# Optimization experiments

Measured on AMD Instinct MI355X. Metric: run time of the kernel, lower is better.

## Reference

```python
import jax, jax.numpy as jnp
import numpy as np

# e3nn normalize2mom constants: 1/sqrt(E[act(z)^2]) for z ~ N(0,1)
_z = np.random.default_rng(0).standard_normal(1_000_000)
_C_SILU = np.float32(1.0 / np.sqrt(np.mean((_z / (1.0 + np.exp(-_z))) ** 2)))
_C_SIGMOID = np.float32(1.0 / np.sqrt(np.mean((1.0 / (1.0 + np.exp(-_z))) ** 2)))

E = 131072
MUL0, MUL1 = 256, 128          # node irreps: 256x0e + 128x1e
RBF = 64
W_NUMEL = 256 + 256 + 128 + 128  # uvu weights in instruction order: A,C,B,D
INV_SQRT3 = np.float32(1.0 / np.sqrt(3.0))
INV_SQRT2 = np.float32(1.0 / np.sqrt(2.0))
INV_SQRT_FAN = np.float32(1.0 / np.sqrt(384.0))  # LinearRS rescale (fan_in=384)


def setup_inputs() -> dict:
    key = jax.random.key(0)
    ks = jax.random.split(key, 8)
    f32 = jnp.float32
    return {
        "node_input": jax.random.normal(ks[0], (E, MUL0 + MUL1 * 3), f32),
        "edge_attr": jax.random.normal(ks[1], (E, 4), f32),        # sh: 1x0e + 1x1e
        "edge_scalars": jax.random.normal(ks[2], (E, RBF), f32),
        "rad_w1": jax.random.normal(ks[3], (RBF, 64), f32) / np.float32(np.sqrt(RBF)),
        "rad_ln_g": jnp.ones((64,), f32),
        "rad_ln_b": jnp.zeros((64,), f32),
        "rad_w2": jax.random.normal(ks[4], (64, W_NUMEL), f32) / np.float32(8.0),
        "rad_offset": jnp.zeros((W_NUMEL,), f32),
        "lin_w0": jax.random.normal(ks[5], (384, 384), f32),
        "lin_b0": jnp.zeros((384,), f32),
        "lin_w1": jax.random.normal(ks[6], (384, MUL1), f32),
    }


def reference(node_input, edge_attr, edge_scalars, rad_w1, rad_ln_g, rad_ln_b,
              rad_w2, rad_offset, lin_w0, lin_b0, lin_w1):
    # --- RadialProfile: Linear(no bias) -> LayerNorm -> SiLU -> Linear(no bias) + offset
    h = edge_scalars @ rad_w1
    mu = jnp.mean(h, axis=-1, keepdims=True)
    var = jnp.var(h, axis=-1, keepdims=True)
    h = (h - mu) * jax.lax.rsqrt(var + 1e-5) * rad_ln_g + rad_ln_b
    h = jax.nn.silu(h)
    w = h @ rad_w2 + rad_offset                        # [E, 768] per-edge DTP weights
    wA, wC, wB, wD = w[:, :256], w[:, 256:512], w[:, 512:640], w[:, 640:]

    x0 = node_input[:, :MUL0]                          # [E,256]  0e
    x1 = node_input[:, MUL0:].reshape(-1, MUL1, 3)     # [E,128,3] 1e
    sh0 = edge_attr[:, 0:1]                            # [E,1]
    sh1 = edge_attr[:, 1:4]                            # [E,3]

    # --- DepthwiseTensorProduct ('uvu', path_weight = sqrt(dim(ir_out)), w3j orthonormal)
    outA = x0 * sh0 * wA                                                # 0e x 0e -> 0e [E,256]
    outB = jnp.einsum('eui,ei->eu', x1, sh1) * INV_SQRT3 * wB           # 1e . 1e -> 0e [E,128]
    outC = (x0 * wC)[:, :, None] * sh1[:, None, :]                      # 0e x 1e -> 1e [E,256,3]
    outD = jnp.cross(x1, sh1[:, None, :]) * INV_SQRT2 * wD[:, :, None]  # 1e x 1e -> 1e [E,128,3]

    d0 = jnp.concatenate([outA, outB], axis=-1)        # [E,384]   0e block (sorted irreps)
    d1 = jnp.concatenate([outC, outD], axis=1)         # [E,384,3] 1e block

    # --- LinearRS: per-irrep linear with 1/sqrt(fan_in) rescale; bias on 0e only
    out0 = d0 @ lin_w0 * INV_SQRT_FAN + lin_b0                       # [E,384] = 256 scalars + 128 gates
    out1 = jnp.einsum('eum,uv->evm', d1, lin_w1) * INV_SQRT_FAN      # [E,128,3] gated 1e

    # --- Gate: normalize2mom(SiLU) on scalars, normalize2mom(sigmoid) gates on 1e
    scalars = _C_SILU * jax.nn.silu(out0[:, :MUL0])
    gates = _C_SIGMOID * jax.nn.sigmoid(out0[:, MUL0:])
    gated = out1 * gates[:, :, None]
    return jnp.concatenate([scalars, gated.reshape(gated.shape[0], -1)], axis=-1)  # [E,640]
```

## Files before the change

### kernel.cpp

```cpp
#include <hip/hip_runtime.h>
#include <stdint.h>

typedef __attribute__((ext_vector_type(8))) short short8;
typedef __attribute__((ext_vector_type(4))) float f32x4;

#define OW1R  0
#define OW2R  4096
#define OW0T  53248
#define OW1CT 200704
#define OW1DT 233472

#define OATTR 0
#define OES   512
#define OHS   4608
#define OD0   8704
#define OH    8704
#define OZC   33280
#define OZD0  49664
#define SMEM_BYTES 74240

static constexpr float C_SILU      = 1.6765390f;
static constexpr float C_SIG       = 1.8462240f;
static constexpr float INV_SQRT3   = 0.5773502691896258f;
static constexpr float INV_SQRT2   = 0.7071067811865476f;
static constexpr float INV_SQRT_FAN= 0.051031036307982884f;

__device__ __forceinline__ short f2bf(float f) {
  union { float f; uint32_t u; } v; v.f = f;
  uint32_t u = v.u;
  u += 0x7FFFu + ((u >> 16) & 1u);
  return (short)(u >> 16);
}

__device__ __forceinline__ f32x4 mfma16(short8 a, short8 b, f32x4 c) {
  return __builtin_amdgcn_mfma_f32_16x16x32_bf16(a, b, c, 0, 0, 0);
}

__device__ __forceinline__ short8 ldF(const short* __restrict__ W, int nkt, int nt, int kt, int lane) {
  return *(const short8*)(W + ((((nt * nkt) + kt) << 6) + lane) * 8);
}

__global__ void prep_weights(const float* __restrict__ rw1, const float* __restrict__ rw2,
                             const float* __restrict__ lw0, const float* __restrict__ lw1,
                             short* __restrict__ ws)
{
  int idx = blockIdx.x * blockDim.x + threadIdx.x;
  int stride = gridDim.x * blockDim.x;
  for (int i = idx; i < 4096; i += stride) {
    int e = i & 7, lane = (i >> 3) & 63, f = i >> 9;
    int kt = f & 1, nt = f >> 1;
    int n = nt * 16 + (lane & 15), k = kt * 32 + ((lane >> 4) << 3) + e;
    ws[OW1R + i] = f2bf(rw1[k * 64 + n]);
  }
  for (int i = idx; i < 49152; i += stride) {
    int e = i & 7, lane = (i >> 3) & 63, f = i >> 9;
    int kt = f & 1, nt = f >> 1;
    int n = nt * 16 + (lane & 15), k = kt * 32 + ((lane >> 4) << 3) + e;
    ws[OW2R + i] = f2bf(rw2[k * 768 + n]);
  }
  for (int i = idx; i < 147456; i += stride) {
    int e = i & 7, lane = (i >> 3) & 63, f = i >> 9;
    int kt = f % 12, nt = f / 12;
    int n = nt * 16 + (lane & 15), k = kt * 32 + ((lane >> 4) << 3) + e;
    ws[OW0T + i] = f2bf(lw0[k * 384 + n] * INV_SQRT_FAN);
  }
  for (int i = idx; i < 32768; i += stride) {
    int e = i & 7, lane = (i >> 3) & 63, f = i >> 9;
    int kt = f & 7, nt = f >> 3;
    int n = nt * 16 + (lane & 15), k = kt * 32 + ((lane >> 4) << 3) + e;
    ws[OW1CT + i] = f2bf(lw1[k * 128 + n] * INV_SQRT_FAN);
  }
  for (int i = idx; i < 16384; i += stride) {
    int e = i & 7, lane = (i >> 3) & 63, f = i >> 9;
    int kt = f & 3, nt = f >> 2;
    int n = nt * 16 + (lane & 15), k = kt * 32 + ((lane >> 4) << 3) + e;
    ws[OW1DT + i] = f2bf(lw1[(256 + k) * 128 + n] * INV_SQRT_FAN);
  }
}

#define SWZ(row, byte) ((byte) ^ ((((row) & 7) << 4) ^ (((row) & 8) << 2)))
#define LDA(base, c2, row, k0) \
  (*(const short8*)(smem + (base) + (row) * (c2) + SWZ(row, (k0) << 1)))
#define STBF(base, c2, row, col, val) \
  (*(short*)(smem + (base) + (row) * (c2) + SWZ(row, (col) << 1)) = f2bf(val))

__global__ __launch_bounds__(256) void fctp_fused(
    const float* __restrict__ node, const float* __restrict__ eattr,
    const float* __restrict__ escal, const float* __restrict__ lng,
    const float* __restrict__ lnb, const float* __restrict__ roff,
    const float* __restrict__ b0v, const short* __restrict__ ws,
    float* __restrict__ out)
{
  __shared__ char smem[SMEM_BYTES];
  const int t = threadIdx.x;
  const int lane = t & 63;
  const int w = t >> 6;
  const int row0 = blockIdx.x << 5;
  const int l15 = lane & 15;
  const int kof = (lane >> 4) << 3;
  const int rb0 = (lane >> 4) << 2;

  float attr_v = 0.f;
  if (t < 128) attr_v = eattr[(size_t)row0 * 4 + t];
  const int pr = t >> 3, pc0 = (t & 7) << 3;
  const float* pesc = escal + (size_t)(row0 + pr) * 64 + pc0;
  float4 ev0 = *(const float4*)pesc;
  float4 ev1 = *(const float4*)(pesc + 4);

  float4 lg0 = *(const float4*)(lng + pc0);
  float4 lg1 = *(const float4*)(lng + pc0 + 4);
  float4 lb0 = *(const float4*)(lnb + pc0);
  float4 lb1 = *(const float4*)(lnb + pc0 + 4);

  float offAr[4], offCr[4], offBr[2], offDr[2];
#pragma unroll
  for (int j = 0; j < 4; ++j) {
    int u = (((w << 2) + j) << 4) + l15;
    offAr[j] = roff[u];
    offCr[j] = roff[256 + u];
  }
#pragma unroll
  for (int j = 0; j < 2; ++j) {
    int u = (((w << 1) + j) << 4) + l15;
    offBr[j] = roff[512 + u];
    offDr[j] = roff[640 + u];
  }

  float x0r[4][2][4];
#pragma unroll
  for (int j = 0; j < 4; ++j) {
    int u = (((w << 2) + j) << 4) + l15;
#pragma unroll
    for (int rt = 0; rt < 2; ++rt)
#pragma unroll
      for (int i = 0; i < 4; ++i)
        x0r[j][rt][i] = node[(size_t)(row0 + rt * 16 + rb0 + i) * 640 + u];
  }
  float x1r[2][2][4][3];
#pragma unroll
  for (int j = 0; j < 2; ++j) {
    int u = (((w << 1) + j) << 4) + l15;
#pragma unroll
    for (int rt = 0; rt < 2; ++rt)
#pragma unroll
      for (int i = 0; i < 4; ++i) {
        const float* xp = node + (size_t)(row0 + rt * 16 + rb0 + i) * 640 + 256 + u * 3;
        x1r[j][rt][i][0] = xp[0];
        x1r[j][rt][i][1] = xp[1];
        x1r[j][rt][i][2] = xp[2];
      }
  }

  {
    if (t < 128) ((float*)(smem + OATTR))[t] = attr_v;
    short8 bv;
    bv[0] = f2bf(ev0.x); bv[1] = f2bf(ev0.y); bv[2] = f2bf(ev0.z); bv[3] = f2bf(ev0.w);
    bv[4] = f2bf(ev1.x); bv[5] = f2bf(ev1.y); bv[6] = f2bf(ev1.z); bv[7] = f2bf(ev1.w);
    *(short8*)(smem + OES + pr * 128 + SWZ(pr, pc0 << 1)) = bv;
  }
  __syncthreads();

  {
    short8 bf0 = ldF(ws + OW1R, 2, w, 0, lane);
    short8 bf1 = ldF(ws + OW1R, 2, w, 1, lane);
    float* sh_h = (float*)(smem + OH);
    int colh = (w << 4) + l15;
#pragma unroll
    for (int rt = 0; rt < 2; ++rt) {
      int r = rt * 16 + l15;
      f32x4 acc = {0.f, 0.f, 0.f, 0.f};
      acc = mfma16(LDA(OES, 128, r, kof), bf0, acc);
      acc = mfma16(LDA(OES, 128, r, 32 + kof), bf1, acc);
      int rb = rt * 16 + rb0;
#pragma unroll
      for (int i = 0; i < 4; ++i) sh_h[(rb + i) * 68 + colh] = acc[i];
    }
  }
  __syncthreads();

  {
    const float* sh_h = (const float*)(smem + OH);
    float vals[8]; float s = 0.f, s2 = 0.f;
#pragma unroll
    for (int j = 0; j < 8; ++j) {
      float v = sh_h[pr * 68 + pc0 + j];
      vals[j] = v; s += v; s2 += v * v;
    }
#pragma unroll
    for (int off = 1; off < 8; off <<= 1) {
      s  += __shfl_xor(s, off, 64);
      s2 += __shfl_xor(s2, off, 64);
    }
    float mu = s * 0.015625f;
    float var = s2 * 0.015625f - mu * mu;
    float rstd = rsqrtf(var + 1e-5f);
    float lg[8] = {lg0.x, lg0.y, lg0.z, lg0.w, lg1.x, lg1.y, lg1.z, lg1.w};
    float lb[8] = {lb0.x, lb0.y, lb0.z, lb0.w, lb1.x, lb1.y, lb1.z, lb1.w};
    short8 hv;
#pragma unroll
    for (int j = 0; j < 8; ++j) {
      float v = (vals[j] - mu) * rstd * lg[j] + lb[j];
      float sv = v / (1.f + __expf(-v));
      hv[j] = f2bf(sv);
    }
    *(short8*)(smem + OHS + pr * 128 + SWZ(pr, pc0 << 1)) = hv;
  }
  __syncthreads();

  {
    const float* attr = (const float*)(smem + OATTR);
    float s0r[2][4], sar[2][4], sbr[2][4], scr[2][4];
#pragma unroll
    for (int rt = 0; rt < 2; ++rt)
#pragma unroll
      for (int i = 0; i < 4; ++i) {
        int row = rt * 16 + rb0 + i;
        s0r[rt][i] = attr[row * 4 + 0];
        sar[rt][i] = attr[row * 4 + 1];
        sbr[rt][i] = attr[row * 4 + 2];
        scr[rt][i] = attr[row * 4 + 3];
      }
    short8 a00 = LDA(OHS, 128, l15, kof);
    short8 a01 = LDA(OHS, 128, l15, 32 + kof);
    short8 a10 = LDA(OHS, 128, 16 + l15, kof);
    short8 a11 = LDA(OHS, 128, 16 + l15, 32 + kof);

#pragma unroll
    for (int j = 0; j < 4; ++j) {
      int ut = (w << 2) + j;
      short8 bA0 = ldF(ws + OW2R, 2, ut, 0, lane);
      short8 bA1 = ldF(ws + OW2R, 2, ut, 1, lane);
      short8 bC0 = ldF(ws + OW2R, 2, ut + 16, 0, lane);
      short8 bC1 = ldF(ws + OW2R, 2, ut + 16, 1, lane);
      int u = (ut << 4) + l15;
#pragma unroll
      for (int rt = 0; rt < 2; ++rt) {
        short8 fa = rt ? a10 : a00, fb = rt ? a11 : a01;
        f32x4 accA = {0.f,0.f,0.f,0.f}, accC = {0.f,0.f,0.f,0.f};
        accA = mfma16(fa, bA0, accA); accA = mfma16(fb, bA1, accA);
        accC = mfma16(fa, bC0, accC); accC = mfma16(fb, bC1, accC);
#pragma unroll
        for (int i = 0; i < 4; ++i) {
          int row = rt * 16 + rb0 + i;
          float x0v = x0r[j][rt][i];
          STBF(OD0, 768, row, u, x0v * s0r[rt][i] * (accA[i] + offAr[j]));
          STBF(OZC, 512, row, u, x0v * (accC[i] + offCr[j]));
        }
      }
    }
#pragma unroll
    for (int j = 0; j < 2; ++j) {
      int ut = (w << 1) + j;
      short8 bB0 = ldF(ws + OW2R, 2, 32 + ut, 0, lane);
      short8 bB1 = ldF(ws + OW2R, 2, 32 + ut, 1, lane);
      short8 bD0 = ldF(ws + OW2R, 2, 40 + ut, 0, lane);
      short8 bD1 = ldF(ws + OW2R, 2, 40 + ut, 1, lane);
      int u = (ut << 4) + l15;
#pragma unroll
      for (int rt = 0; rt < 2; ++rt) {
        short8 fa = rt ? a10 : a00, fb = rt ? a11 : a01;
        f32x4 accB = {0.f,0.f,0.f,0.f}, accD = {0.f,0.f,0.f,0.f};
        accB = mfma16(fa, bB0, accB); accB = mfma16(fb, bB1, accB);
        accD = mfma16(fa, bD0, accD); accD = mfma16(fb, bD1, accD);
#pragma unroll
        for (int i = 0; i < 4; ++i) {
          int row = rt * 16 + rb0 + i;
          float xa = x1r[j][rt][i][0], xb = x1r[j][rt][i][1], xc = x1r[j][rt][i][2];
          float sa = sar[rt][i], sb = sbr[rt][i], sc = scr[rt][i];
          float wB = accB[i] + offBr[j], wD = accD[i] + offDr[j];
          STBF(OD0, 768, row, 256 + u,
               (xa * sa + xb * sb + xc * sc) * INV_SQRT3 * wB);
          float zd = wD * INV_SQRT2;
          STBF(OZD0,          256, row, u, xa * zd);
          STBF(OZD0 + 8192,   256, row, u, xb * zd);
          STBF(OZD0 + 16384,  256, row, u, xc * zd);
        }
      }
    }
  }
  __syncthreads();


#pragma unroll
  for (int cp = 0; cp < 2; ++cp) {
    f32x4 sacc[2][2];
#pragma unroll
    for (int q = 0; q < 2; ++q)
#pragma unroll
      for (int rt = 0; rt < 2; ++rt) sacc[q][rt] = (f32x4){0.f, 0.f, 0.f, 0.f};
#pragma unroll
    for (int kt = 0; kt < 12; ++kt) {
      int k0 = kt * 32 + kof;
      short8 Af0 = LDA(OD0, 768, l15, k0);
      short8 Af1 = LDA(OD0, 768, 16 + l15, k0);
      short8 Bf0 = ldF(ws + OW0T, 12, (w << 2) + 2 * cp,     kt, lane);
      short8 Bf1 = ldF(ws + OW0T, 12, (w << 2) + 2 * cp + 1, kt, lane);
      sacc[0][0] = mfma16(Af0, Bf0, sacc[0][0]);
      sacc[0][1] = mfma16(Af1, Bf0, sacc[0][1]);
      sacc[1][0] = mfma16(Af0, Bf1, sacc[1][0]);
      sacc[1][1] = mfma16(Af1, Bf1, sacc[1][1]);
    }
#pragma unroll
    for (int q = 0; q < 2; ++q) {
      int col = (((w << 2) + 2 * cp + q) << 4) + l15;
      float bias = b0v[col];
#pragma unroll
      for (int rt = 0; rt < 2; ++rt) {
#pragma unroll
        for (int i = 0; i < 4; ++i) {
          float v = sacc[q][rt][i] + bias;
          float sv = v / (1.f + __expf(-v));
          out[(size_t)(row0 + rt * 16 + rb0 + i) * 640 + col] = C_SILU * sv;
        }
      }
    }
  }

  f32x4 gacc[2][2];
#pragma unroll
  for (int j = 0; j < 2; ++j)
#pragma unroll
    for (int rt = 0; rt < 2; ++rt) gacc[j][rt] = (f32x4){0.f, 0.f, 0.f, 0.f};
#pragma unroll
  for (int kt = 0; kt < 12; ++kt) {
    int k0 = kt * 32 + kof;
    short8 Af0 = LDA(OD0, 768, l15, k0);
    short8 Af1 = LDA(OD0, 768, 16 + l15, k0);
    short8 Bg0 = ldF(ws + OW0T, 12, 16 + (w << 1),     kt, lane);
    short8 Bg1 = ldF(ws + OW0T, 12, 16 + (w << 1) + 1, kt, lane);
    gacc[0][0] = mfma16(Af0, Bg0, gacc[0][0]);
    gacc[0][1] = mfma16(Af1, Bg0, gacc[0][1]);
    gacc[1][0] = mfma16(Af0, Bg1, gacc[1][0]);
    gacc[1][1] = mfma16(Af1, Bg1, gacc[1][1]);
  }

  f32x4 ycacc[2][2];
#pragma unroll
  for (int j = 0; j < 2; ++j)
#pragma unroll
    for (int rt = 0; rt < 2; ++rt) ycacc[j][rt] = (f32x4){0.f, 0.f, 0.f, 0.f};
  {
    short8 Az[2][8];
#pragma unroll
    for (int kt = 0; kt < 8; ++kt) {
      int k0 = kt * 32 + kof;
      Az[0][kt] = LDA(OZC, 512, l15, k0);
      Az[1][kt] = LDA(OZC, 512, 16 + l15, k0);
    }
#pragma unroll
    for (int j = 0; j < 2; ++j) {
      int vt = (w << 1) + j;
      short8 Bfr[8];
#pragma unroll
      for (int kt = 0; kt < 8; ++kt) Bfr[kt] = ldF(ws + OW1CT, 8, vt, kt, lane);
#pragma unroll
      for (int kt = 0; kt < 8; ++kt) {
        ycacc[j][0] = mfma16(Az[0][kt], Bfr[kt], ycacc[j][0]);
        ycacc[j][1] = mfma16(Az[1][kt], Bfr[kt], ycacc[j][1]);
      }
    }
  }

  f32x4 pacc[3][2][2];
#pragma unroll
  for (int m = 0; m < 3; ++m)
#pragma unroll
    for (int j = 0; j < 2; ++j)
#pragma unroll
      for (int rt = 0; rt < 2; ++rt) pacc[m][j][rt] = (f32x4){0.f, 0.f, 0.f, 0.f};
#pragma unroll
  for (int m = 0; m < 3; ++m) {
    short8 Az[2][4];
#pragma unroll
    for (int kt4 = 0; kt4 < 4; ++kt4) {
      int k0 = kt4 * 32 + kof;
      Az[0][kt4] = LDA(OZD0 + m * 8192, 256, l15, k0);
      Az[1][kt4] = LDA(OZD0 + m * 8192, 256, 16 + l15, k0);
    }
#pragma unroll
    for (int j = 0; j < 2; ++j) {
      int vt = (w << 1) + j;
      short8 Bfr[4];
#pragma unroll
      for (int kt4 = 0; kt4 < 4; ++kt4) Bfr[kt4] = ldF(ws + OW1DT, 4, vt, kt4, lane);
#pragma unroll
      for (int kt4 = 0; kt4 < 4; ++kt4) {
        pacc[m][j][0] = mfma16(Az[0][kt4], Bfr[kt4], pacc[m][j][0]);
        pacc[m][j][1] = mfma16(Az[1][kt4], Bfr[kt4], pacc[m][j][1]);
      }
    }
  }

  {
    const float* attr = (const float*)(smem + OATTR);
#pragma unroll
    for (int j = 0; j < 2; ++j) {
      int v = (((w << 1) + j) << 4) + l15;
      float bias = b0v[256 + v];
#pragma unroll
      for (int rt = 0; rt < 2; ++rt) {
#pragma unroll
        for (int i = 0; i < 4; ++i) {
          int row = rt * 16 + rb0 + i;
          float gate = C_SIG / (1.f + __expf(-(gacc[j][rt][i] + bias)));
          float ra = attr[row * 4 + 1], rb = attr[row * 4 + 2], rc = attr[row * 4 + 3];
          float yc = ycacc[j][rt][i];
          float q0 = pacc[0][j][rt][i], q1 = pacc[1][j][rt][i], q2 = pacc[2][j][rt][i];
          float o0 = ra * yc + (rc * q1 - rb * q2);
          float o1 = rb * yc + (ra * q2 - rc * q0);
          float o2 = rc * yc + (rb * q0 - ra * q1);
          float* op = out + (size_t)(row0 + row) * 640 + 256 + v * 3;
          op[0] = o0 * gate; op[1] = o1 * gate; op[2] = o2 * gate;
        }
      }
    }
  }
}

extern "C" void kernel_launch(void* const* d_in, const int* in_sizes, int n_in,
                              void* d_out, int out_size, void* d_ws, size_t ws_size,
                              hipStream_t stream) {
  const float* node_input   = (const float*)d_in[0];
  const float* edge_attr    = (const float*)d_in[1];
  const float* edge_scalars = (const float*)d_in[2];
  const float* rad_w1       = (const float*)d_in[3];
  const float* rad_ln_g     = (const float*)d_in[4];
  const float* rad_ln_b     = (const float*)d_in[5];
  const float* rad_w2       = (const float*)d_in[6];
  const float* rad_offset   = (const float*)d_in[7];
  const float* lin_w0       = (const float*)d_in[8];
  const float* lin_b0       = (const float*)d_in[9];
  const float* lin_w1       = (const float*)d_in[10];
  short* wsb = (short*)d_ws;
  float* out = (float*)d_out;

  prep_weights<<<256, 256, 0, stream>>>(rad_w1, rad_w2, lin_w0, lin_w1, wsb);
  fctp_fused<<<131072 / 32, 256, 0, stream>>>(node_input, edge_attr, edge_scalars,
                                              rad_ln_g, rad_ln_b, rad_offset,
                                              lin_b0, wsb, out);
}
```

Before: 302.2 us.

## Shrink LDS footprint by reusing one buffer for the three D-path components

Cuts the shared memory per block by staging the three 1e cross-product components through a single reused LDS buffer (aliased onto the early ES/HS region), and computes the D-path MFMAs right after the radial stage. Edge attributes now come straight from global into registers instead of through LDS. The goal is more resident blocks per CU through lower LDS use. The cost is extra __syncthreads barriers between component passes and longer-lived registers for zd, pacc and the attributes, which could push register pressure up.

```diff
diff --git a/kernel.cpp b/kernel.cpp
--- a/kernel.cpp
+++ b/kernel.cpp
@@ -10,14 +10,13 @@
 #define OW1CT 200704
 #define OW1DT 233472
 
-#define OATTR 0
-#define OES   512
-#define OHS   4608
-#define OD0   8704
-#define OH    8704
-#define OZC   33280
-#define OZD0  49664
-#define SMEM_BYTES 74240
+#define OES   0
+#define OHS   4096
+#define OD0   8192
+#define OH    8192
+#define OZC   32768
+#define OZDS  0
+#define SMEM_BYTES 49152
 
 static constexpr float C_SILU      = 1.6765390f;
 static constexpr float C_SIG       = 1.8462240f;
@@ -100,8 +99,6 @@
   const int kof = (lane >> 4) << 3;
   const int rb0 = (lane >> 4) << 2;
 
-  float attr_v = 0.f;
-  if (t < 128) attr_v = eattr[(size_t)row0 * 4 + t];
   const int pr = t >> 3, pc0 = (t & 7) << 3;
   const float* pesc = escal + (size_t)(row0 + pr) * 64 + pc0;
   float4 ev0 = *(const float4*)pesc;
@@ -152,7 +149,6 @@
   }
 
   {
-    if (t < 128) ((float*)(smem + OATTR))[t] = attr_v;
     short8 bv;
     bv[0] = f2bf(ev0.x); bv[1] = f2bf(ev0.y); bv[2] = f2bf(ev0.z); bv[3] = f2bf(ev0.w);
     bv[4] = f2bf(ev1.x); bv[5] = f2bf(ev1.y); bv[6] = f2bf(ev1.z); bv[7] = f2bf(ev1.w);
@@ -207,79 +203,123 @@
   }
   __syncthreads();
 
-  {
-    const float* attr = (const float*)(smem + OATTR);
-    float s0r[2][4], sar[2][4], sbr[2][4], scr[2][4];
-#pragma unroll
-    for (int rt = 0; rt < 2; ++rt)
+  float s0r[2][4], sar[2][4], sbr[2][4], scr[2][4];
+#pragma unroll
+  for (int rt = 0; rt < 2; ++rt)
+#pragma unroll
+    for (int i = 0; i < 4; ++i) {
+      int row = rt * 16 + rb0 + i;
+      float4 att = *(const float4*)(eattr + (size_t)(row0 + row) * 4);
+      s0r[rt][i] = att.x;
+      sar[rt][i] = att.y;
+      sbr[rt][i] = att.z;
+      scr[rt][i] = att.w;
+    }
+  short8 a00 = LDA(OHS, 128, l15, kof);
+  short8 a01 = LDA(OHS, 128, l15, 32 + kof);
+  short8 a10 = LDA(OHS, 128, 16 + l15, kof);
+  short8 a11 = LDA(OHS, 128, 16 + l15, 32 + kof);
+
+#pragma unroll
+  for (int j = 0; j < 4; ++j) {
+    int ut = (w << 2) + j;
+    short8 bA0 = ldF(ws + OW2R, 2, ut, 0, lane);
+    short8 bA1 = ldF(ws + OW2R, 2, ut, 1, lane);
+    short8 bC0 = ldF(ws + OW2R, 2, ut + 16, 0, lane);
+    short8 bC1 = ldF(ws + OW2R, 2, ut + 16, 1, lane);
+    int u = (ut << 4) + l15;
+#pragma unroll
+    for (int rt = 0; rt < 2; ++rt) {
+      short8 fa = rt ? a10 : a00, fb = rt ? a11 : a01;
+      f32x4 accA = {0.f,0.f,0.f,0.f}, accC = {0.f,0.f,0.f,0.f};
+      accA = mfma16(fa, bA0, accA); accA = mfma16(fb, bA1, accA);
+      accC = mfma16(fa, bC0, accC); accC = mfma16(fb, bC1, accC);
 #pragma unroll
       for (int i = 0; i < 4; ++i) {
         int row = rt * 16 + rb0 + i;
-        s0r[rt][i] = attr[row * 4 + 0];
-        sar[rt][i] = attr[row * 4 + 1];
-        sbr[rt][i] = attr[row * 4 + 2];
-        scr[rt][i] = attr[row * 4 + 3];
-      }
-    short8 a00 = LDA(OHS, 128, l15, kof);
-    short8 a01 = LDA(OHS, 128, l15, 32 + kof);
-    short8 a10 = LDA(OHS, 128, 16 + l15, kof);
-    short8 a11 = LDA(OHS, 128, 16 + l15, 32 + kof);
-
-#pragma unroll
-    for (int j = 0; j < 4; ++j) {
-      int ut = (w << 2) + j;
-      short8 bA0 = ldF(ws + OW2R, 2, ut, 0, lane);
-      short8 bA1 = ldF(ws + OW2R, 2, ut, 1, lane);
-      short8 bC0 = ldF(ws + OW2R, 2, ut + 16, 0, lane);
-      short8 bC1 = ldF(ws + OW2R, 2, ut + 16, 1, lane);
-      int u = (ut << 4) + l15;
-#pragma unroll
-      for (int rt = 0; rt < 2; ++rt) {
-        short8 fa = rt ? a10 : a00, fb = rt ? a11 : a01;
-        f32x4 accA = {0.f,0.f,0.f,0.f}, accC = {0.f,0.f,0.f,0.f};
-        accA = mfma16(fa, bA0, accA); accA = mfma16(fb, bA1, accA);
-        accC = mfma16(fa, bC0, accC); accC = mfma16(fb, bC1, accC);
-#pragma unroll
-        for (int i = 0; i < 4; ++i) {
-          int row = rt * 16 + rb0 + i;
-          float x0v = x0r[j][rt][i];
-          STBF(OD0, 768, row, u, x0v * s0r[rt][i] * (accA[i] + offAr[j]));
-          STBF(OZC, 512, row, u, x0v * (accC[i] + offCr[j]));
-        }
-      }
+        float x0v = x0r[j][rt][i];
+        STBF(OD0, 768, row, u, x0v * s0r[rt][i] * (accA[i] + offAr[j]));
+        STBF(OZC, 512, row, u, x0v * (accC[i] + offCr[j]));
+      }
+    }
+  }
+  __syncthreads();
+
+  float zd[2][2][4];
+#pragma unroll
+  for (int j = 0; j < 2; ++j) {
+    int ut = (w << 1) + j;
+    short8 bB0 = ldF(ws + OW2R, 2, 32 + ut, 0, lane);
+    short8 bB1 = ldF(ws + OW2R, 2, 32 + ut, 1, lane);
+    short8 bD0 = ldF(ws + OW2R, 2, 40 + ut, 0, lane);
+    short8 bD1 = ldF(ws + OW2R, 2, 40 + ut, 1, lane);
+    int u = (ut << 4) + l15;
+#pragma unroll
+    for (int rt = 0; rt < 2; ++rt) {
+      short8 fa = rt ? a10 : a00, fb = rt ? a11 : a01;
+      f32x4 accB = {0.f,0.f,0.f,0.f}, accD = {0.f,0.f,0.f,0.f};
+      accB = mfma16(fa, bB0, accB); accB = mfma16(fb, bB1, accB);
+      accD = mfma16(fa, bD0, accD); accD = mfma16(fb, bD1, accD);
+#pragma unroll
+      for (int i = 0; i < 4; ++i) {
+        int row = rt * 16 + rb0 + i;
+        float xa = x1r[j][rt][i][0], xb = x1r[j][rt][i][1], xc = x1r[j][rt][i][2];
+        float wB = accB[i] + offBr[j];
+        STBF(OD0, 768, row, 256 + u,
+             (xa * sar[rt][i] + xb * sbr[rt][i] + xc * scr[rt][i]) * INV_SQRT3 * wB);
+        float z = (accD[i] + offDr[j]) * INV_SQRT2;
+        zd[j][rt][i] = z;
+        STBF(OZDS, 256, row, u, xa * z);
+      }
+    }
+  }
+  __syncthreads();
+
+  f32x4 pacc[3][2][2];
+#pragma unroll
+  for (int m = 0; m < 3; ++m)
+#pragma unroll
+    for (int j = 0; j < 2; ++j)
+#pragma unroll
+      for (int rt = 0; rt < 2; ++rt) pacc[m][j][rt] = (f32x4){0.f, 0.f, 0.f, 0.f};
+
+#pragma unroll
+  for (int m = 0; m < 3; ++m) {
+    if (m > 0) {
+      __syncthreads();
+#pragma unroll
+      for (int j = 0; j < 2; ++j) {
+        int u = (((w << 1) + j) << 4) + l15;
+#pragma unroll
+        for (int rt = 0; rt < 2; ++rt)
+#pragma unroll
+          for (int i = 0; i < 4; ++i) {
+            int row = rt * 16 + rb0 + i;
+            STBF(OZDS, 256, row, u, x1r[j][rt][i][m] * zd[j][rt][i]);
+          }
+      }
+      __syncthreads();
+    }
+    short8 Az[2][4];
+#pragma unroll
+    for (int kt4 = 0; kt4 < 4; ++kt4) {
+      int k0 = kt4 * 32 + kof;
+      Az[0][kt4] = LDA(OZDS, 256, l15, k0);
+      Az[1][kt4] = LDA(OZDS, 256, 16 + l15, k0);
     }
 #pragma unroll
     for (int j = 0; j < 2; ++j) {
-      int ut = (w << 1) + j;
-      short8 bB0 = ldF(ws + OW2R, 2, 32 + ut, 0, lane);
-      short8 bB1 = ldF(ws + OW2R, 2, 32 + ut, 1, lane);
-      short8 bD0 = ldF(ws + OW2R, 2, 40 + ut, 0, lane);
-      short8 bD1 = ldF(ws + OW2R, 2, 40 + ut, 1, lane);
-      int u = (ut << 4) + l15;
-#pragma unroll
-      for (int rt = 0; rt < 2; ++rt) {
-        short8 fa = rt ? a10 : a00, fb = rt ? a11 : a01;
-        f32x4 accB = {0.f,0.f,0.f,0.f}, accD = {0.f,0.f,0.f,0.f};
-        accB = mfma16(fa, bB0, accB); accB = mfma16(fb, bB1, accB);
-        accD = mfma16(fa, bD0, accD); accD = mfma16(fb, bD1, accD);
-#pragma unroll
-        for (int i = 0; i < 4; ++i) {
-          int row = rt * 16 + rb0 + i;
-          float xa = x1r[j][rt][i][0], xb = x1r[j][rt][i][1], xc = x1r[j][rt][i][2];
-          float sa = sar[rt][i], sb = sbr[rt][i], sc = scr[rt][i];
-          float wB = accB[i] + offBr[j], wD = accD[i] + offDr[j];
-          STBF(OD0, 768, row, 256 + u,
-               (xa * sa + xb * sb + xc * sc) * INV_SQRT3 * wB);
-          float zd = wD * INV_SQRT2;
-          STBF(OZD0,          256, row, u, xa * zd);
-          STBF(OZD0 + 8192,   256, row, u, xb * zd);
-          STBF(OZD0 + 16384,  256, row, u, xc * zd);
-        }
-      }
-    }
-  }
-  __syncthreads();
-
+      int vt = (w << 1) + j;
+      short8 Bfr[4];
+#pragma unroll
+      for (int kt4 = 0; kt4 < 4; ++kt4) Bfr[kt4] = ldF(ws + OW1DT, 4, vt, kt4, lane);
+#pragma unroll
+      for (int kt4 = 0; kt4 < 4; ++kt4) {
+        pacc[m][j][0] = mfma16(Az[0][kt4], Bfr[kt4], pacc[m][j][0]);
+        pacc[m][j][1] = mfma16(Az[1][kt4], Bfr[kt4], pacc[m][j][1]);
+      }
+    }
+  }
 
 #pragma unroll
   for (int cp = 0; cp < 2; ++cp) {
@@ -361,38 +401,7 @@
     }
   }
 
-  f32x4 pacc[3][2][2];
-#pragma unroll
-  for (int m = 0; m < 3; ++m)
-#pragma unroll
-    for (int j = 0; j < 2; ++j)
-#pragma unroll
-      for (int rt = 0; rt < 2; ++rt) pacc[m][j][rt] = (f32x4){0.f, 0.f, 0.f, 0.f};
-#pragma unroll
-  for (int m = 0; m < 3; ++m) {
-    short8 Az[2][4];
-#pragma unroll
-    for (int kt4 = 0; kt4 < 4; ++kt4) {
-      int k0 = kt4 * 32 + kof;
-      Az[0][kt4] = LDA(OZD0 + m * 8192, 256, l15, k0);
-      Az[1][kt4] = LDA(OZD0 + m * 8192, 256, 16 + l15, k0);
-    }
-#pragma unroll
-    for (int j = 0; j < 2; ++j) {
-      int vt = (w << 1) + j;
-      short8 Bfr[4];
-#pragma unroll
-      for (int kt4 = 0; kt4 < 4; ++kt4) Bfr[kt4] = ldF(ws + OW1DT, 4, vt, kt4, lane);
-#pragma unroll
-      for (int kt4 = 0; kt4 < 4; ++kt4) {
-        pacc[m][j][0] = mfma16(Az[0][kt4], Bfr[kt4], pacc[m][j][0]);
-        pacc[m][j][1] = mfma16(Az[1][kt4], Bfr[kt4], pacc[m][j][1]);
-      }
-    }
-  }
-
   {
-    const float* attr = (const float*)(smem + OATTR);
 #pragma unroll
     for (int j = 0; j < 2; ++j) {
       int v = (((w << 1) + j) << 4) + l15;
@@ -403,7 +412,7 @@
         for (int i = 0; i < 4; ++i) {
           int row = rt * 16 + rb0 + i;
           float gate = C_SIG / (1.f + __expf(-(gacc[j][rt][i] + bias)));
-          float ra = attr[row * 4 + 1], rb = attr[row * 4 + 2], rc = attr[row * 4 + 3];
+          float ra = sar[rt][i], rb = sbr[rt][i], rc = scr[rt][i];
           float yc = ycacc[j][rt][i];
           float q0 = pacc[0][j][rt][i], q1 = pacc[1][j][rt][i], q2 = pacc[2][j][rt][i];
           float o0 = ra * yc + (rc * q1 - rb * q2);
```

After: 423.8 us. +40.3%, slower.
